# Kernel optimization log

Hardware: AMD Instinct MI355X
Metric: run time of the kernel (lower is better)

The kernel has to match this reference:

```python
import jax, jax.numpy as jnp
import numpy as np

SR = 16000
HOP = 256
MIN_F0 = 50.0
MAX_F0 = 500.0
MIN_PERIOD = SR // 500          # 32
MAX_PERIOD = SR // 50           # 320
FRAME_LEN = HOP * 2             # 512
LAG_END = min(MAX_PERIOD, FRAME_LEN // 2)  # 256 -> lags 32..255 (224 lags)


def setup_inputs() -> dict:
    key = jax.random.key(0)
    waveform = jax.random.normal(key, (64, 1, 163840), dtype=jnp.float32)
    return {"waveform": waveform}


def reference(waveform):
    B, C, T = waveform.shape
    x = waveform[:, 0, :]  # (B, T)
    pad = FRAME_LEN // 2
    xpad = jnp.pad(x, ((0, 0), (pad, pad)), mode='reflect')
    n_frames = (T + 2 * pad - FRAME_LEN) // HOP + 1  # = T//HOP + 1
    # frame extraction (equivalent to unfold(frame_length, hop))
    idx = np.arange(n_frames)[:, None] * HOP + np.arange(FRAME_LEN)[None, :]
    frames = xpad[:, idx]  # (B, F, L)
    # L2-normalize each frame
    norm = jnp.sqrt(jnp.sum(frames * frames, axis=-1, keepdims=True))
    xn = frames / (norm + 1e-8)
    # zero-pad right so xn[t] * xz[t+p] reproduces frame[:L-p] * frame[p:]
    xz = jnp.pad(xn, ((0, 0), (0, 0), (0, FRAME_LEN)))
    lags = jnp.arange(MIN_PERIOD, LAG_END)

    def step(carry, p):
        sl = jax.lax.dynamic_slice_in_dim(xz, p, FRAME_LEN, axis=-1)
        return carry, jnp.sum(xn * sl, axis=-1)  # (B, F)

    _, ac = jax.lax.scan(step, None, lags)  # (P, B, F)
    max_idx = jnp.argmax(ac, axis=0)  # (B, F)
    period = max_idx.astype(jnp.float32) + MIN_PERIOD
    f0 = SR / (period + 1e-8)
    return jnp.clip(f0, MIN_F0, MAX_F0)  # (B, F)
```

## Files before the change

kernel.cpp:

```cpp
#include <hip/hip_runtime.h>


#define SR_F 16000.0f
#define HOP 256
#define FRAME_LEN 512
#define PAD 256
#define T_LEN 163840
#define N_FRAMES 641
#define MIN_PERIOD 32
#define N_LAGS 224
#define WPB 4
#define CP 408
#define L0_OFF 1632
#define L1_OFF 2032
#define WAVE_DW 2432
#define NC 15

typedef _Float16 half8 __attribute__((ext_vector_type(8)));
typedef float floatx4 __attribute__((ext_vector_type(4)));
typedef unsigned int uint2v __attribute__((ext_vector_type(2)));

__device__ __forceinline__ int swz(int q) { return q ^ ((q >> 3) & 7); }

__device__ __forceinline__ unsigned int pkh(float a, float b) {
    unsigned short ha = __builtin_bit_cast(unsigned short, (_Float16)a);
    unsigned short hb = __builtin_bit_cast(unsigned short, (_Float16)b);
    return (unsigned int)ha | ((unsigned int)hb << 16);
}

#define DPP_XOR1 0xB1
#define DPP_XOR2 0x4E
#define DPP_ROR4 0x124
#define DPP_ROR8 0x128

template <int CTRL> __device__ __forceinline__ int dppi(int x) {
    return __builtin_amdgcn_update_dpp(0, x, CTRL, 0xF, 0xF, false);
}
template <int CTRL> __device__ __forceinline__ float dppf(float x) {
    return __builtin_bit_cast(float, dppi<CTRL>(__builtin_bit_cast(int, x)));
}

__device__ __forceinline__ uint2v pl16sw(unsigned int x, bool sel) {
#if __has_builtin(__builtin_amdgcn_permlane16_swap)
    (void)sel;
    return __builtin_amdgcn_permlane16_swap(x, x, false, false);
#else
    unsigned int p = (unsigned int)__shfl_xor((int)x, 16);
    uint2v r; r[0] = sel ? p : x; r[1] = sel ? x : p; return r;
#endif
}
__device__ __forceinline__ uint2v pl32sw(unsigned int x, bool sel) {
#if __has_builtin(__builtin_amdgcn_permlane32_swap)
    (void)sel;
    return __builtin_amdgcn_permlane32_swap(x, x, false, false);
#else
    unsigned int p = (unsigned int)__shfl_xor((int)x, 32);
    uint2v r; r[0] = sel ? p : x; r[1] = sel ? x : p; return r;
#endif
}

__device__ __forceinline__ float wave_sum(float x, bool oddrow, bool hihalf) {
    x += dppf<DPP_XOR1>(x);
    x += dppf<DPP_XOR2>(x);
    x += dppf<DPP_ROR4>(x);
    x += dppf<DPP_ROR8>(x);
    uint2v p = pl16sw(__builtin_bit_cast(unsigned int, x), oddrow);
    x = __builtin_bit_cast(float, p[0]) + __builtin_bit_cast(float, p[1]);
    p = pl32sw(__builtin_bit_cast(unsigned int, x), hihalf);
    x = __builtin_bit_cast(float, p[0]) + __builtin_bit_cast(float, p[1]);
    return x;
}

__device__ __forceinline__
void top2_comb(float& v1, int& i1, float& v2, float ov1, int oi1, float ov2) {
    bool take = (ov1 > v1) || (ov1 == v1 && oi1 < i1);
    float lose = take ? v1 : ov1;
    if (take) { v1 = ov1; i1 = oi1; }
    v2 = fmaxf(fmaxf(v2, ov2), lose);
}

template <int CTRL> __device__ __forceinline__
void top2_dpp(float& v1, int& i1, float& v2) {
    float ov1 = dppf<CTRL>(v1);
    int   oi1 = dppi<CTRL>(i1);
    float ov2 = dppf<CTRL>(v2);
    top2_comb(v1, i1, v2, ov1, oi1, ov2);
}

__device__ __forceinline__
void top2_full(floatx4 acc, int qd, int nn, bool oddrow, bool hihalf,
               float& v1, int& i1, float& v2) {
    v1 = acc[0];
    i1 = 64*qd + nn;
    v2 = -__builtin_inff();
    #pragma unroll
    for (int r = 1; r < 4; ++r) {
        float cv = (4*qd + r < 14) ? acc[r] : -__builtin_inff();
        bool take = (cv > v1);
        float lose = take ? v1 : cv;
        if (take) { v1 = cv; i1 = 64*qd + 16*r + nn; }
        v2 = fmaxf(v2, lose);
    }
    top2_dpp<DPP_XOR1>(v1, i1, v2);
    top2_dpp<DPP_XOR2>(v1, i1, v2);
    top2_dpp<DPP_ROR4>(v1, i1, v2);
    top2_dpp<DPP_ROR8>(v1, i1, v2);
    {
        uint2v a = pl16sw(__builtin_bit_cast(unsigned int, v1), oddrow);
        uint2v b = pl16sw((unsigned int)i1, oddrow);
        uint2v c = pl16sw(__builtin_bit_cast(unsigned int, v2), oddrow);
        float ov1 = __builtin_bit_cast(float, oddrow ? a[0] : a[1]);
        int   oi1 = (int)(oddrow ? b[0] : b[1]);
        float ov2 = __builtin_bit_cast(float, oddrow ? c[0] : c[1]);
        top2_comb(v1, i1, v2, ov1, oi1, ov2);
    }
    {
        uint2v a = pl32sw(__builtin_bit_cast(unsigned int, v1), hihalf);
        uint2v b = pl32sw((unsigned int)i1, hihalf);
        uint2v c = pl32sw(__builtin_bit_cast(unsigned int, v2), hihalf);
        float ov1 = __builtin_bit_cast(float, hihalf ? a[0] : a[1]);
        int   oi1 = (int)(hihalf ? b[0] : b[1]);
        float ov2 = __builtin_bit_cast(float, hihalf ? c[0] : c[1]);
        top2_comb(v1, i1, v2, ov1, oi1, ov2);
    }
}

__device__ __forceinline__ void write_hi4(unsigned int* c0_, unsigned int* c1_,
                                          unsigned int* c2_, unsigned int* c3_,
                                          unsigned int u10, unsigned int u11,
                                          unsigned int u20, unsigned int u21,
                                          int lane) {
    *(unsigned long long*)(c0_ + 120 + 2*lane) =
        ((unsigned long long)u11 << 32) | u10;
    *(unsigned long long*)(c0_ + 248 + 2*lane) =
        ((unsigned long long)u21 << 32) | u20;
    unsigned int a  = __shfl(u10, (lane + 1) & 63);
    unsigned int bb = __shfl(u20, (lane + 1) & 63);
    unsigned int n1 = (lane == 63) ? bb : a;
    unsigned int n2 = (lane == 63) ? 0u : bb;
    unsigned int o10 = (u10 >> 16) | (u11 << 16);
    unsigned int o11 = (u11 >> 16) | (n1 << 16);
    unsigned int o20 = (u20 >> 16) | (u21 << 16);
    unsigned int o21 = (u21 >> 16) | (n2 << 16);
    *(unsigned long long*)(c1_ + 120 + 2*lane) =
        ((unsigned long long)o11 << 32) | o10;
    *(unsigned long long*)(c1_ + 248 + 2*lane) =
        ((unsigned long long)o21 << 32) | o20;
    c2_[119 + 2*lane] = u10; c2_[120 + 2*lane] = u11;
    c2_[247 + 2*lane] = u20; c2_[248 + 2*lane] = u21;
    c3_[119 + 2*lane] = o10; c3_[120 + 2*lane] = o11;
    c3_[247 + 2*lane] = o20; c3_[248 + 2*lane] = o21;
}

__device__ __forceinline__ void write_lo2(unsigned int* l0_, unsigned int* l1_,
                                          unsigned int u10, unsigned int u11,
                                          unsigned int u20, unsigned int u21,
                                          int lane) {
    *(unsigned long long*)(l0_ + 120 + 2*lane) =
        ((unsigned long long)u11 << 32) | u10;
    *(unsigned long long*)(l0_ + 248 + 2*lane) =
        ((unsigned long long)u21 << 32) | u20;
    unsigned int a  = __shfl(u10, (lane + 1) & 63);
    unsigned int bb = __shfl(u20, (lane + 1) & 63);
    unsigned int n1 = (lane == 63) ? bb : a;
    unsigned int n2 = (lane == 63) ? 0u : bb;
    *(unsigned long long*)(l1_ + 120 + 2*lane) =
        ((unsigned long long)(((u11 >> 16) | (n1 << 16))) << 32) |
        ((u10 >> 16) | (u11 << 16));
    *(unsigned long long*)(l1_ + 248 + 2*lane) =
        ((unsigned long long)(((u21 >> 16) | (n2 << 16))) << 32) |
        ((u20 >> 16) | (u21 << 16));
}

__global__ __launch_bounds__(256, 4) void f0_kernel(const float* __restrict__ wav,
                                                    float* __restrict__ out) {
    __shared__ unsigned int yw[WPB][WAVE_DW];

    const int tid  = threadIdx.x;
    const int wv   = tid >> 6;
    const int lane = tid & 63;
    unsigned int* c0p = yw[wv];
    unsigned int* c1p = c0p + CP;
    unsigned int* c2p = c0p + 2*CP;
    unsigned int* c3p = c0p + 3*CP;
    unsigned int* l0p = c0p + L0_OFF;
    unsigned int* l1p = c0p + L1_OFF;

    const int xcd = blockIdx.x & 7;
    const int idx = blockIdx.x >> 3;
    const int bf  = (xcd * 1282 + idx) * WPB + wv;
    const int b   = bf / N_FRAMES;
    const int f   = bf - b * N_FRAMES;
    const float* __restrict__ x = wav + (size_t)b * T_LEN;
    const int base = f * HOP - PAD;
    const bool fast = (f != 0 && f != N_FRAMES - 1);

    const int qd = lane >> 4;
    const int nn = lane & 15;
    const int par = nn & 1;
    const int wA0 = 120 + 4*qd - 8*nn;
    const unsigned int* bhp = c0p + CP*(nn & 3) + 136 + 4*qd + 2*(nn >> 2);
    const int wB0old = 136 + 4*qd + ((nn - par) >> 1);
    const int seg = lane & 15;
    const bool s0 = (seg & 1), s1 = (seg & 2), s2 = (seg & 4), s3 = (seg & 8);
    const bool oddrow = (lane & 16) != 0;
    const bool hihalf = (lane & 32) != 0;

    float4 c1, c2;
    if (fast) {
        const float4* g4 = (const float4*)(x + base);
        c1 = g4[lane];
        c2 = g4[lane + 64];
    }
    for (int d = lane; d < 120; d += 64) { c0p[d] = 0u; l0p[d] = 0u; }
    if (lane < 28) {
        int d = 374 + lane;
        c0p[d] = 0u; c1p[d] = 0u; c2p[d] = 0u; c3p[d] = 0u;
        l0p[d] = 0u; l1p[d] = 0u;
    }

    float qen = 0.0f;
    if (fast) {
        qen = c1.x*c1.x + c1.y*c1.y + c1.z*c1.z + c1.w*c1.w
            + c2.x*c2.x + c2.y*c2.y + c2.z*c2.z + c2.w*c2.w;
        write_hi4(c0p, c1p, c2p, c3p, pkh(c1.x, c1.y), pkh(c1.z, c1.w),
                                      pkh(c2.x, c2.y), pkh(c2.z, c2.w), lane);
    } else {
        for (int t = lane; t < FRAME_LEN; t += 64) {
            int idxr = base + t;
            if (idxr < 0) idxr = -idxr;
            if (idxr >= T_LEN) idxr = 2 * (T_LEN - 1) - idxr;
            float v = x[idxr];
            qen = __builtin_fmaf(v, v, qen);
            unsigned short h = __builtin_bit_cast(unsigned short, (_Float16)v);
            ((unsigned short*)c0p)[240 + t] = h;
            ((unsigned short*)c1p)[239 + t] = h;
            ((unsigned short*)c2p)[238 + t] = h;
            ((unsigned short*)c3p)[237 + t] = h;
        }
    }
    __threadfence_block();

    qen = wave_sum(qen, oddrow, hihalf);

    floatx4 acc0 = {0.f, 0.f, 0.f, 0.f};
    floatx4 acc1 = {0.f, 0.f, 0.f, 0.f};
    #pragma unroll
    for (int c = 0; c < NC; ++c) {
        uint4 au = *(const uint4*)(c0p + (wA0 + 16*c));
        unsigned long long bl = *(const unsigned long long*)(bhp + 16*c);
        unsigned long long br = *(const unsigned long long*)(bhp + 16*c + 2);
        uint4 bu; bu.x = (unsigned int)bl; bu.y = (unsigned int)(bl >> 32);
        bu.z = (unsigned int)br; bu.w = (unsigned int)(br >> 32);
        if (c & 1)
            acc1 = __builtin_amdgcn_mfma_f32_16x16x32_f16(
                __builtin_bit_cast(half8, au), __builtin_bit_cast(half8, bu),
                acc1, 0, 0, 0);
        else
            acc0 = __builtin_amdgcn_mfma_f32_16x16x32_f16(
                __builtin_bit_cast(half8, au), __builtin_bit_cast(half8, bu),
                acc0, 0, 0, 0);
    }
    floatx4 acc = acc0 + acc1;

    float v1, v2; int i1;
    top2_full(acc, qd, nn, oddrow, hihalf, v1, i1, v2);

    const float E1 = 9.765625e-4f * qen + 0.05f;
    if (v1 - v2 > 2.0f * E1) {
        if (lane == 0) {
            float period = (float)(i1 + MIN_PERIOD);
            float f0 = SR_F / (period + 1e-8f);
            out[bf] = fminf(fmaxf(f0, 50.0f), 500.0f);
        }
        return;
    }

    if (fast) {
        float l0 = c1.x - (float)(_Float16)c1.x;
        float l1 = c1.y - (float)(_Float16)c1.y;
        float l2 = c1.z - (float)(_Float16)c1.z;
        float l3 = c1.w - (float)(_Float16)c1.w;
        float l4 = c2.x - (float)(_Float16)c2.x;
        float l5 = c2.y - (float)(_Float16)c2.y;
        float l6 = c2.z - (float)(_Float16)c2.z;
        float l7 = c2.w - (float)(_Float16)c2.w;
        write_lo2(l0p, l1p, pkh(l0, l1), pkh(l2, l3),
                            pkh(l4, l5), pkh(l6, l7), lane);
    } else {
        for (int t = lane; t < FRAME_LEN; t += 64) {
            int idxr = base + t;
            if (idxr < 0) idxr = -idxr;
            if (idxr >= T_LEN) idxr = 2 * (T_LEN - 1) - idxr;
            float v = x[idxr];
            float l = v - (float)(_Float16)v;
            unsigned short h = __builtin_bit_cast(unsigned short, (_Float16)l);
            ((unsigned short*)l0p)[240 + t] = h;
            ((unsigned short*)l1p)[239 + t] = h;
        }
    }
    __threadfence_block();

    const unsigned int* ybl = par ? l1p : l0p;
    #pragma unroll
    for (int c = 0; c < NC; ++c) {
        uint4 au = *(const uint4*)(c0p + (wA0 + 16*c));
        const unsigned int* p = ybl + (wB0old + 16*c);
        uint4 bu; bu.x = p[0]; bu.y = p[1]; bu.z = p[2]; bu.w = p[3];
        acc = __builtin_amdgcn_mfma_f32_16x16x32_f16(
            __builtin_bit_cast(half8, au), __builtin_bit_cast(half8, bu),
            acc, 0, 0, 0);
    }
    #pragma unroll
    for (int c = 0; c < NC; ++c) {
        uint4 au = *(const uint4*)(l0p + (wA0 + 16*c));
        unsigned long long bl = *(const unsigned long long*)(bhp + 16*c);
        unsigned long long br = *(const unsigned long long*)(bhp + 16*c + 2);
        uint4 bu; bu.x = (unsigned int)bl; bu.y = (unsigned int)(bl >> 32);
        bu.z = (unsigned int)br; bu.w = (unsigned int)(br >> 32);
        acc = __builtin_amdgcn_mfma_f32_16x16x32_f16(
            __builtin_bit_cast(half8, au), __builtin_bit_cast(half8, bu),
            acc, 0, 0, 0);
    }

    top2_full(acc, qd, nn, oddrow, hihalf, v1, i1, v2);

    const float E2 = 1.0e-4f * qen + 0.02f;
    if (v1 - v2 > 2.0f * E2) {
        if (lane == 0) {
            float period = (float)(i1 + MIN_PERIOD);
            float f0 = SR_F / (period + 1e-8f);
            out[bf] = fminf(fmaxf(f0, 50.0f), 500.0f);
        }
        return;
    }

    float* sw = (float*)c0p;
    if (fast) {
        const float4* g4 = (const float4*)(x + base);
        ((float4*)sw)[swz(lane)]      = g4[lane];
        ((float4*)sw)[swz(lane + 64)] = g4[lane + 64];
        if (lane < 16) ((float4*)sw)[swz(lane + 128)] = make_float4(0.f,0.f,0.f,0.f);
    } else {
        for (int t = lane; t < FRAME_LEN; t += 64) {
            int idxr = base + t;
            if (idxr < 0) idxr = -idxr;
            if (idxr >= T_LEN) idxr = 2 * (T_LEN - 1) - idxr;
            sw[(swz(t >> 2) << 2) | (t & 3)] = x[idxr];
        }
        int t = FRAME_LEN + lane;
        sw[(swz(t >> 2) << 2) | (t & 3)] = 0.0f;
    }
    __threadfence_block();

    const float4* s4 = (const float4*)sw;
    double dtot[4];
    #pragma unroll
    for (int r = 0; r < 4; ++r) {
        const int g  = (r << 2) + qd;
        const int p0 = MIN_PERIOD + (g << 4);
        double dacc[16];
        #pragma unroll
        for (int j = 0; j < 16; ++j) dacc[j] = 0.0;
        if (g < 14) {
            const int n16 = (FRAME_LEN - p0 + 15) >> 4;
            #pragma unroll
            for (int k = 0; k < 2; ++k) {
                const int ch = seg + (k << 4);
                if (ch < n16) {
                    const int t  = ch << 4;
                    const int qa = t >> 2;
                    const int qw = (t + p0) >> 2;
                    float a[16], w[32];
                    #pragma unroll
                    for (int u = 0; u < 4; ++u) {
                        float4 v = s4[swz(qa + u)];
                        a[4*u+0]=v.x; a[4*u+1]=v.y; a[4*u+2]=v.z; a[4*u+3]=v.w;
                    }
                    #pragma unroll
                    for (int u = 0; u < 8; ++u) {
                        float4 v = s4[swz(qw + u)];
                        w[4*u+0]=v.x; w[4*u+1]=v.y; w[4*u+2]=v.z; w[4*u+3]=v.w;
                    }
                    #pragma unroll
                    for (int j = 0; j < 16; ++j) {
                        #pragma unroll
                        for (int i = 0; i < 16; ++i)
                            dacc[j] = fma((double)a[i], (double)w[i + j], dacc[j]);
                    }
                }
            }
        }
        double u8[8], u4[4], u2[2], dtotal;
        #pragma unroll
        for (int i = 0; i < 8; ++i) {
            double lo = dacc[2*i], hi = dacc[2*i+1];
            double keep = s0 ? hi : lo, send = s0 ? lo : hi;
            u8[i] = keep + __shfl_xor(send, 1);
        }
        #pragma unroll
        for (int i = 0; i < 4; ++i) {
            double lo = u8[2*i], hi = u8[2*i+1];
            double keep = s1 ? hi : lo, send = s1 ? lo : hi;
            u4[i] = keep + __shfl_xor(send, 2);
        }
        #pragma unroll
        for (int i = 0; i < 2; ++i) {
            double lo = u4[2*i], hi = u4[2*i+1];
            double keep = s2 ? hi : lo, send = s2 ? lo : hi;
            u2[i] = keep + __shfl_xor(send, 4);
        }
        {
            double lo = u2[0], hi = u2[1];
            double keep = s3 ? hi : lo, send = s3 ? lo : hi;
            dtotal = keep + __shfl_xor(send, 8);
        }
        dtot[r] = ((r << 6) + lane < N_LAGS) ? dtotal : -__builtin_inf();
    }
    double dv1 = dtot[0];
    int    di1 = lane;
    #pragma unroll
    for (int r = 1; r < 4; ++r) {
        double c = dtot[r];
        if (c > dv1) { dv1 = c; di1 = (r << 6) + lane; }
    }
    #pragma unroll
    for (int m = 1; m < 64; m <<= 1) {
        double o = __shfl_xor(dv1, m);
        int   oi = __shfl_xor(di1, m);
        if (o > dv1 || (o == dv1 && oi < di1)) { dv1 = o; di1 = oi; }
    }
    if (lane == 0) {
        float period = (float)(di1 + MIN_PERIOD);
        float f0 = SR_F / (period + 1e-8f);
        out[bf] = fminf(fmaxf(f0, 50.0f), 500.0f);
    }
}

extern "C" void kernel_launch(void* const* d_in, const int* in_sizes, int n_in,
                              void* d_out, int out_size, void* d_ws, size_t ws_size,
                              hipStream_t stream) {
    const float* wav = (const float*)d_in[0];
    float* out = (float*)d_out;
    const int n_blocks = (64 * N_FRAMES) / WPB;
    f0_kernel<<<n_blocks, 256, 0, stream>>>(wav, out);
}
```

Before: 131.0 us.

## Split tiered f0 search into screening kernel plus compacted refinement kernel

Splits the single kernel into three launches: a counter reset, a tier-1 fp16 MFMA screening kernel that processes 8 frames per wave and emits confident results, and a tier-2/3 kernel that handles only the ambiguous frames gathered into a global work list by atomic append. Divergent slow-path waves no longer hold occupancy alongside fast-path waves, and tier-1 can run with less LDS and higher occupancy. In exchange it adds two extra kernel launches, a global atomic per ambiguous frame, and reloads the waveform for refined frames.

```diff
diff --git a/kernel.cpp b/kernel.cpp
--- a/kernel.cpp
+++ b/kernel.cpp
@@ -7,18 +7,27 @@
 #define PAD 256
 #define T_LEN 163840
 #define N_FRAMES 641
+#define TOTAL (64 * N_FRAMES)
 #define MIN_PERIOD 32
 #define N_LAGS 224
 #define WPB 4
 #define CP 408
+#define T1_DW (4 * CP)
 #define L0_OFF 1632
 #define L1_OFF 2032
-#define WAVE_DW 2432
+#define T23_DW 2432
 #define NC 15
+#define T1_BLOCKS 1282
+#define NF 8
+#define T23_BLOCKS 768
+#define T23_STRIDE (T23_BLOCKS * WPB)
 
 typedef _Float16 half8 __attribute__((ext_vector_type(8)));
 typedef float floatx4 __attribute__((ext_vector_type(4)));
 typedef unsigned int uint2v __attribute__((ext_vector_type(2)));
+
+__device__ unsigned int g_cnt2;
+__device__ unsigned int g_lst2[TOTAL];
 
 __device__ __forceinline__ int swz(int q) { return q ^ ((q >> 3) & 7); }
 
@@ -172,9 +181,120 @@
         ((u20 >> 16) | (u21 << 16));
 }
 
-__global__ __launch_bounds__(256, 4) void f0_kernel(const float* __restrict__ wav,
-                                                    float* __restrict__ out) {
-    __shared__ unsigned int yw[WPB][WAVE_DW];
+__device__ __forceinline__ void emit(float* out, int bf, int i1) {
+    float period = (float)(i1 + MIN_PERIOD);
+    float f0 = SR_F / (period + 1e-8f);
+    out[bf] = fminf(fmaxf(f0, 50.0f), 500.0f);
+}
+
+__global__ void f0_zero() {
+    if (threadIdx.x == 0) g_cnt2 = 0u;
+}
+
+__global__ __launch_bounds__(256, 4) void f0_t1(const float* __restrict__ wav,
+                                                float* __restrict__ out) {
+    __shared__ unsigned int yw[WPB][T1_DW];
+
+    const int tid  = threadIdx.x;
+    const int wv   = tid >> 6;
+    const int lane = tid & 63;
+    unsigned int* c0p = yw[wv];
+    unsigned int* c1p = c0p + CP;
+    unsigned int* c2p = c0p + 2*CP;
+    unsigned int* c3p = c0p + 3*CP;
+
+    const int xcd = blockIdx.x & 7;
+    const int bi  = blockIdx.x >> 3;
+    const int cblk = (xcd < 2 ? xcd * 161 : 322 + (xcd - 2) * 160) + bi;
+    const int bf0  = (cblk * WPB + wv) * NF;
+
+    const int qd = lane >> 4;
+    const int nn = lane & 15;
+    const int wA0 = 120 + 4*qd - 8*nn;
+    const unsigned int* bhp = c0p + CP*(nn & 3) + 136 + 4*qd + 2*(nn >> 2);
+    const bool oddrow = (lane & 16) != 0;
+    const bool hihalf = (lane & 32) != 0;
+
+    for (int d = lane; d < 120; d += 64) c0p[d] = 0u;
+    if (lane < 28) {
+        int d = 374 + lane;
+        c0p[d] = 0u; c1p[d] = 0u; c2p[d] = 0u; c3p[d] = 0u;
+    }
+
+    for (int j = 0; j < NF; ++j) {
+        const int bf = bf0 + j;
+        const int b  = bf / N_FRAMES;
+        const int f  = bf - b * N_FRAMES;
+        const float* __restrict__ x = wav + (size_t)b * T_LEN;
+        const int base = f * HOP - PAD;
+        const bool fast = (f != 0 && f != N_FRAMES - 1);
+
+        __threadfence_block();
+        float qen = 0.0f;
+        if (fast) {
+            const float4* g4 = (const float4*)(x + base);
+            float4 c1 = g4[lane];
+            float4 c2 = g4[lane + 64];
+            qen = c1.x*c1.x + c1.y*c1.y + c1.z*c1.z + c1.w*c1.w
+                + c2.x*c2.x + c2.y*c2.y + c2.z*c2.z + c2.w*c2.w;
+            write_hi4(c0p, c1p, c2p, c3p, pkh(c1.x, c1.y), pkh(c1.z, c1.w),
+                                          pkh(c2.x, c2.y), pkh(c2.z, c2.w), lane);
+        } else {
+            for (int t = lane; t < FRAME_LEN; t += 64) {
+                int idxr = base + t;
+                if (idxr < 0) idxr = -idxr;
+                if (idxr >= T_LEN) idxr = 2 * (T_LEN - 1) - idxr;
+                float v = x[idxr];
+                qen = __builtin_fmaf(v, v, qen);
+                unsigned short h = __builtin_bit_cast(unsigned short, (_Float16)v);
+                ((unsigned short*)c0p)[240 + t] = h;
+                ((unsigned short*)c1p)[239 + t] = h;
+                ((unsigned short*)c2p)[238 + t] = h;
+                ((unsigned short*)c3p)[237 + t] = h;
+            }
+        }
+        __threadfence_block();
+
+        qen = wave_sum(qen, oddrow, hihalf);
+
+        floatx4 acc0 = {0.f, 0.f, 0.f, 0.f};
+        floatx4 acc1 = {0.f, 0.f, 0.f, 0.f};
+        #pragma unroll
+        for (int c = 0; c < NC; ++c) {
+            uint4 au = *(const uint4*)(c0p + (wA0 + 16*c));
+            unsigned long long bl = *(const unsigned long long*)(bhp + 16*c);
+            unsigned long long br = *(const unsigned long long*)(bhp + 16*c + 2);
+            uint4 bu; bu.x = (unsigned int)bl; bu.y = (unsigned int)(bl >> 32);
+            bu.z = (unsigned int)br; bu.w = (unsigned int)(br >> 32);
+            if (c & 1)
+                acc1 = __builtin_amdgcn_mfma_f32_16x16x32_f16(
+                    __builtin_bit_cast(half8, au), __builtin_bit_cast(half8, bu),
+                    acc1, 0, 0, 0);
+            else
+                acc0 = __builtin_amdgcn_mfma_f32_16x16x32_f16(
+                    __builtin_bit_cast(half8, au), __builtin_bit_cast(half8, bu),
+                    acc0, 0, 0, 0);
+        }
+        floatx4 acc = acc0 + acc1;
+
+        float v1, v2; int i1;
+        top2_full(acc, qd, nn, oddrow, hihalf, v1, i1, v2);
+
+        const float E1 = 9.765625e-4f * qen + 0.05f;
+        if (lane == 0) {
+            if (v1 - v2 > 2.0f * E1) {
+                emit(out, bf, i1);
+            } else {
+                unsigned int ii = atomicAdd(&g_cnt2, 1u);
+                g_lst2[ii] = (unsigned int)bf;
+            }
+        }
+    }
+}
+
+__global__ __launch_bounds__(256, 2) void f0_t23(const float* __restrict__ wav,
+                                                 float* __restrict__ out) {
+    __shared__ unsigned int yw[WPB][T23_DW];
 
     const int tid  = threadIdx.x;
     const int wv   = tid >> 6;
@@ -185,15 +305,6 @@
     unsigned int* c3p = c0p + 3*CP;
     unsigned int* l0p = c0p + L0_OFF;
     unsigned int* l1p = c0p + L1_OFF;
-
-    const int xcd = blockIdx.x & 7;
-    const int idx = blockIdx.x >> 3;
-    const int bf  = (xcd * 1282 + idx) * WPB + wv;
-    const int b   = bf / N_FRAMES;
-    const int f   = bf - b * N_FRAMES;
-    const float* __restrict__ x = wav + (size_t)b * T_LEN;
-    const int base = f * HOP - PAD;
-    const bool fast = (f != 0 && f != N_FRAMES - 1);
 
     const int qd = lane >> 4;
     const int nn = lane & 15;
@@ -206,234 +317,225 @@
     const bool oddrow = (lane & 16) != 0;
     const bool hihalf = (lane & 32) != 0;
 
-    float4 c1, c2;
-    if (fast) {
-        const float4* g4 = (const float4*)(x + base);
-        c1 = g4[lane];
-        c2 = g4[lane + 64];
-    }
-    for (int d = lane; d < 120; d += 64) { c0p[d] = 0u; l0p[d] = 0u; }
+    for (int d = lane; d < 120; d += 64) l0p[d] = 0u;
     if (lane < 28) {
         int d = 374 + lane;
-        c0p[d] = 0u; c1p[d] = 0u; c2p[d] = 0u; c3p[d] = 0u;
-        l0p[d] = 0u; l1p[d] = 0u;
-    }
-
-    float qen = 0.0f;
-    if (fast) {
-        qen = c1.x*c1.x + c1.y*c1.y + c1.z*c1.z + c1.w*c1.w
-            + c2.x*c2.x + c2.y*c2.y + c2.z*c2.z + c2.w*c2.w;
-        write_hi4(c0p, c1p, c2p, c3p, pkh(c1.x, c1.y), pkh(c1.z, c1.w),
-                                      pkh(c2.x, c2.y), pkh(c2.z, c2.w), lane);
-    } else {
-        for (int t = lane; t < FRAME_LEN; t += 64) {
-            int idxr = base + t;
-            if (idxr < 0) idxr = -idxr;
-            if (idxr >= T_LEN) idxr = 2 * (T_LEN - 1) - idxr;
-            float v = x[idxr];
-            qen = __builtin_fmaf(v, v, qen);
-            unsigned short h = __builtin_bit_cast(unsigned short, (_Float16)v);
-            ((unsigned short*)c0p)[240 + t] = h;
-            ((unsigned short*)c1p)[239 + t] = h;
-            ((unsigned short*)c2p)[238 + t] = h;
-            ((unsigned short*)c3p)[237 + t] = h;
-        }
-    }
-    __threadfence_block();
-
-    qen = wave_sum(qen, oddrow, hihalf);
-
-    floatx4 acc0 = {0.f, 0.f, 0.f, 0.f};
-    floatx4 acc1 = {0.f, 0.f, 0.f, 0.f};
-    #pragma unroll
-    for (int c = 0; c < NC; ++c) {
-        uint4 au = *(const uint4*)(c0p + (wA0 + 16*c));
-        unsigned long long bl = *(const unsigned long long*)(bhp + 16*c);
-        unsigned long long br = *(const unsigned long long*)(bhp + 16*c + 2);
-        uint4 bu; bu.x = (unsigned int)bl; bu.y = (unsigned int)(bl >> 32);
-        bu.z = (unsigned int)br; bu.w = (unsigned int)(br >> 32);
-        if (c & 1)
-            acc1 = __builtin_amdgcn_mfma_f32_16x16x32_f16(
+        c1p[d] = 0u; c2p[d] = 0u; c3p[d] = 0u; l0p[d] = 0u; l1p[d] = 0u;
+    }
+
+    const unsigned int cnt = g_cnt2;
+    for (unsigned int it = blockIdx.x * WPB + wv; it < cnt; it += T23_STRIDE) {
+        const int bf = (int)g_lst2[it];
+        const int b  = bf / N_FRAMES;
+        const int f  = bf - b * N_FRAMES;
+        const float* __restrict__ x = wav + (size_t)b * T_LEN;
+        const int base = f * HOP - PAD;
+        const bool fast = (f != 0 && f != N_FRAMES - 1);
+
+        __threadfence_block();
+        for (int d = lane; d < 120; d += 64) c0p[d] = 0u;
+        if (lane < 28) c0p[374 + lane] = 0u;
+
+        float4 c1, c2;
+        float qen = 0.0f;
+        if (fast) {
+            const float4* g4 = (const float4*)(x + base);
+            c1 = g4[lane];
+            c2 = g4[lane + 64];
+            qen = c1.x*c1.x + c1.y*c1.y + c1.z*c1.z + c1.w*c1.w
+                + c2.x*c2.x + c2.y*c2.y + c2.z*c2.z + c2.w*c2.w;
+            write_hi4(c0p, c1p, c2p, c3p, pkh(c1.x, c1.y), pkh(c1.z, c1.w),
+                                          pkh(c2.x, c2.y), pkh(c2.z, c2.w), lane);
+        } else {
+            for (int t = lane; t < FRAME_LEN; t += 64) {
+                int idxr = base + t;
+                if (idxr < 0) idxr = -idxr;
+                if (idxr >= T_LEN) idxr = 2 * (T_LEN - 1) - idxr;
+                float v = x[idxr];
+                qen = __builtin_fmaf(v, v, qen);
+                unsigned short h = __builtin_bit_cast(unsigned short, (_Float16)v);
+                ((unsigned short*)c0p)[240 + t] = h;
+                ((unsigned short*)c1p)[239 + t] = h;
+                ((unsigned short*)c2p)[238 + t] = h;
+                ((unsigned short*)c3p)[237 + t] = h;
+            }
+        }
+        __threadfence_block();
+
+        qen = wave_sum(qen, oddrow, hihalf);
+
+        floatx4 acc0 = {0.f, 0.f, 0.f, 0.f};
+        floatx4 acc1 = {0.f, 0.f, 0.f, 0.f};
+        #pragma unroll
+        for (int c = 0; c < NC; ++c) {
+            uint4 au = *(const uint4*)(c0p + (wA0 + 16*c));
+            unsigned long long bl = *(const unsigned long long*)(bhp + 16*c);
+            unsigned long long br = *(const unsigned long long*)(bhp + 16*c + 2);
+            uint4 bu; bu.x = (unsigned int)bl; bu.y = (unsigned int)(bl >> 32);
+            bu.z = (unsigned int)br; bu.w = (unsigned int)(br >> 32);
+            if (c & 1)
+                acc1 = __builtin_amdgcn_mfma_f32_16x16x32_f16(
+                    __builtin_bit_cast(half8, au), __builtin_bit_cast(half8, bu),
+                    acc1, 0, 0, 0);
+            else
+                acc0 = __builtin_amdgcn_mfma_f32_16x16x32_f16(
+                    __builtin_bit_cast(half8, au), __builtin_bit_cast(half8, bu),
+                    acc0, 0, 0, 0);
+        }
+        floatx4 acc = acc0 + acc1;
+
+        if (fast) {
+            float l0 = c1.x - (float)(_Float16)c1.x;
+            float l1 = c1.y - (float)(_Float16)c1.y;
+            float l2 = c1.z - (float)(_Float16)c1.z;
+            float l3 = c1.w - (float)(_Float16)c1.w;
+            float l4 = c2.x - (float)(_Float16)c2.x;
+            float l5 = c2.y - (float)(_Float16)c2.y;
+            float l6 = c2.z - (float)(_Float16)c2.z;
+            float l7 = c2.w - (float)(_Float16)c2.w;
+            write_lo2(l0p, l1p, pkh(l0, l1), pkh(l2, l3),
+                                pkh(l4, l5), pkh(l6, l7), lane);
+        } else {
+            for (int t = lane; t < FRAME_LEN; t += 64) {
+                int idxr = base + t;
+                if (idxr < 0) idxr = -idxr;
+                if (idxr >= T_LEN) idxr = 2 * (T_LEN - 1) - idxr;
+                float v = x[idxr];
+                float l = v - (float)(_Float16)v;
+                unsigned short h = __builtin_bit_cast(unsigned short, (_Float16)l);
+                ((unsigned short*)l0p)[240 + t] = h;
+                ((unsigned short*)l1p)[239 + t] = h;
+            }
+        }
+        __threadfence_block();
+
+        const unsigned int* ybl = par ? l1p : l0p;
+        #pragma unroll
+        for (int c = 0; c < NC; ++c) {
+            uint4 au = *(const uint4*)(c0p + (wA0 + 16*c));
+            const unsigned int* p = ybl + (wB0old + 16*c);
+            uint4 bu; bu.x = p[0]; bu.y = p[1]; bu.z = p[2]; bu.w = p[3];
+            acc = __builtin_amdgcn_mfma_f32_16x16x32_f16(
                 __builtin_bit_cast(half8, au), __builtin_bit_cast(half8, bu),
-                acc1, 0, 0, 0);
-        else
-            acc0 = __builtin_amdgcn_mfma_f32_16x16x32_f16(
+                acc, 0, 0, 0);
+        }
+        #pragma unroll
+        for (int c = 0; c < NC; ++c) {
+            uint4 au = *(const uint4*)(l0p + (wA0 + 16*c));
+            unsigned long long bl = *(const unsigned long long*)(bhp + 16*c);
+            unsigned long long br = *(const unsigned long long*)(bhp + 16*c + 2);
+            uint4 bu; bu.x = (unsigned int)bl; bu.y = (unsigned int)(bl >> 32);
+            bu.z = (unsigned int)br; bu.w = (unsigned int)(br >> 32);
+            acc = __builtin_amdgcn_mfma_f32_16x16x32_f16(
                 __builtin_bit_cast(half8, au), __builtin_bit_cast(half8, bu),
-                acc0, 0, 0, 0);
-    }
-    floatx4 acc = acc0 + acc1;
-
-    float v1, v2; int i1;
-    top2_full(acc, qd, nn, oddrow, hihalf, v1, i1, v2);
-
-    const float E1 = 9.765625e-4f * qen + 0.05f;
-    if (v1 - v2 > 2.0f * E1) {
-        if (lane == 0) {
-            float period = (float)(i1 + MIN_PERIOD);
-            float f0 = SR_F / (period + 1e-8f);
-            out[bf] = fminf(fmaxf(f0, 50.0f), 500.0f);
-        }
-        return;
-    }
-
-    if (fast) {
-        float l0 = c1.x - (float)(_Float16)c1.x;
-        float l1 = c1.y - (float)(_Float16)c1.y;
-        float l2 = c1.z - (float)(_Float16)c1.z;
-        float l3 = c1.w - (float)(_Float16)c1.w;
-        float l4 = c2.x - (float)(_Float16)c2.x;
-        float l5 = c2.y - (float)(_Float16)c2.y;
-        float l6 = c2.z - (float)(_Float16)c2.z;
-        float l7 = c2.w - (float)(_Float16)c2.w;
-        write_lo2(l0p, l1p, pkh(l0, l1), pkh(l2, l3),
-                            pkh(l4, l5), pkh(l6, l7), lane);
-    } else {
-        for (int t = lane; t < FRAME_LEN; t += 64) {
-            int idxr = base + t;
-            if (idxr < 0) idxr = -idxr;
-            if (idxr >= T_LEN) idxr = 2 * (T_LEN - 1) - idxr;
-            float v = x[idxr];
-            float l = v - (float)(_Float16)v;
-            unsigned short h = __builtin_bit_cast(unsigned short, (_Float16)l);
-            ((unsigned short*)l0p)[240 + t] = h;
-            ((unsigned short*)l1p)[239 + t] = h;
-        }
-    }
-    __threadfence_block();
-
-    const unsigned int* ybl = par ? l1p : l0p;
-    #pragma unroll
-    for (int c = 0; c < NC; ++c) {
-        uint4 au = *(const uint4*)(c0p + (wA0 + 16*c));
-        const unsigned int* p = ybl + (wB0old + 16*c);
-        uint4 bu; bu.x = p[0]; bu.y = p[1]; bu.z = p[2]; bu.w = p[3];
-        acc = __builtin_amdgcn_mfma_f32_16x16x32_f16(
-            __builtin_bit_cast(half8, au), __builtin_bit_cast(half8, bu),
-            acc, 0, 0, 0);
-    }
-    #pragma unroll
-    for (int c = 0; c < NC; ++c) {
-        uint4 au = *(const uint4*)(l0p + (wA0 + 16*c));
-        unsigned long long bl = *(const unsigned long long*)(bhp + 16*c);
-        unsigned long long br = *(const unsigned long long*)(bhp + 16*c + 2);
-        uint4 bu; bu.x = (unsigned int)bl; bu.y = (unsigned int)(bl >> 32);
-        bu.z = (unsigned int)br; bu.w = (unsigned int)(br >> 32);
-        acc = __builtin_amdgcn_mfma_f32_16x16x32_f16(
-            __builtin_bit_cast(half8, au), __builtin_bit_cast(half8, bu),
-            acc, 0, 0, 0);
-    }
-
-    top2_full(acc, qd, nn, oddrow, hihalf, v1, i1, v2);
-
-    const float E2 = 1.0e-4f * qen + 0.02f;
-    if (v1 - v2 > 2.0f * E2) {
-        if (lane == 0) {
-            float period = (float)(i1 + MIN_PERIOD);
-            float f0 = SR_F / (period + 1e-8f);
-            out[bf] = fminf(fmaxf(f0, 50.0f), 500.0f);
-        }
-        return;
-    }
-
-    float* sw = (float*)c0p;
-    if (fast) {
-        const float4* g4 = (const float4*)(x + base);
-        ((float4*)sw)[swz(lane)]      = g4[lane];
-        ((float4*)sw)[swz(lane + 64)] = g4[lane + 64];
-        if (lane < 16) ((float4*)sw)[swz(lane + 128)] = make_float4(0.f,0.f,0.f,0.f);
-    } else {
-        for (int t = lane; t < FRAME_LEN; t += 64) {
-            int idxr = base + t;
-            if (idxr < 0) idxr = -idxr;
-            if (idxr >= T_LEN) idxr = 2 * (T_LEN - 1) - idxr;
-            sw[(swz(t >> 2) << 2) | (t & 3)] = x[idxr];
-        }
-        int t = FRAME_LEN + lane;
-        sw[(swz(t >> 2) << 2) | (t & 3)] = 0.0f;
-    }
-    __threadfence_block();
-
-    const float4* s4 = (const float4*)sw;
-    double dtot[4];
-    #pragma unroll
-    for (int r = 0; r < 4; ++r) {
-        const int g  = (r << 2) + qd;
-        const int p0 = MIN_PERIOD + (g << 4);
-        double dacc[16];
-        #pragma unroll
-        for (int j = 0; j < 16; ++j) dacc[j] = 0.0;
-        if (g < 14) {
-            const int n16 = (FRAME_LEN - p0 + 15) >> 4;
+                acc, 0, 0, 0);
+        }
+
+        float v1, v2; int i1;
+        top2_full(acc, qd, nn, oddrow, hihalf, v1, i1, v2);
+
+        const float E2 = 1.0e-4f * qen + 0.02f;
+        if (v1 - v2 > 2.0f * E2) {
+            if (lane == 0) emit(out, bf, i1);
+            continue;
+        }
+
+        float* sw = (float*)c0p;
+        if (fast) {
+            const float4* g4 = (const float4*)(x + base);
+            ((float4*)sw)[swz(lane)]      = g4[lane];
+            ((float4*)sw)[swz(lane + 64)] = g4[lane + 64];
+            if (lane < 16) ((float4*)sw)[swz(lane + 128)] = make_float4(0.f,0.f,0.f,0.f);
+        } else {
+            for (int t = lane; t < FRAME_LEN; t += 64) {
+                int idxr = base + t;
+                if (idxr < 0) idxr = -idxr;
+                if (idxr >= T_LEN) idxr = 2 * (T_LEN - 1) - idxr;
+                sw[(swz(t >> 2) << 2) | (t & 3)] = x[idxr];
+            }
+            int t = FRAME_LEN + lane;
+            sw[(swz(t >> 2) << 2) | (t & 3)] = 0.0f;
+        }
+        __threadfence_block();
+
+        const float4* s4 = (const float4*)sw;
+        double dtot[4];
+        #pragma unroll
+        for (int r = 0; r < 4; ++r) {
+            const int g  = (r << 2) + qd;
+            const int p0 = MIN_PERIOD + (g << 4);
+            double dacc[16];
             #pragma unroll
-            for (int k = 0; k < 2; ++k) {
-                const int ch = seg + (k << 4);
-                if (ch < n16) {
-                    const int t  = ch << 4;
-                    const int qa = t >> 2;
-                    const int qw = (t + p0) >> 2;
-                    float a[16], w[32];
-                    #pragma unroll
-                    for (int u = 0; u < 4; ++u) {
-                        float4 v = s4[swz(qa + u)];
-                        a[4*u+0]=v.x; a[4*u+1]=v.y; a[4*u+2]=v.z; a[4*u+3]=v.w;
-                    }
-                    #pragma unroll
-                    for (int u = 0; u < 8; ++u) {
-                        float4 v = s4[swz(qw + u)];
-                        w[4*u+0]=v.x; w[4*u+1]=v.y; w[4*u+2]=v.z; w[4*u+3]=v.w;
-                    }
-                    #pragma unroll
-                    for (int j = 0; j < 16; ++j) {
+            for (int j = 0; j < 16; ++j) dacc[j] = 0.0;
+            if (g < 14) {
+                const int n16 = (FRAME_LEN - p0 + 15) >> 4;
+                #pragma unroll
+                for (int k = 0; k < 2; ++k) {
+                    const int ch = seg + (k << 4);
+                    if (ch < n16) {
+                        const int t  = ch << 4;
+                        const int qa = t >> 2;
+                        const int qw = (t + p0) >> 2;
+                        float a[16], w[32];
                         #pragma unroll
-                        for (int i = 0; i < 16; ++i)
-                            dacc[j] = fma((double)a[i], (double)w[i + j], dacc[j]);
+                        for (int u = 0; u < 4; ++u) {
+                            float4 v = s4[swz(qa + u)];
+                            a[4*u+0]=v.x; a[4*u+1]=v.y; a[4*u+2]=v.z; a[4*u+3]=v.w;
+                        }
+                        #pragma unroll
+                        for (int u = 0; u < 8; ++u) {
+                            float4 v = s4[swz(qw + u)];
+                            w[4*u+0]=v.x; w[4*u+1]=v.y; w[4*u+2]=v.z; w[4*u+3]=v.w;
+                        }
+                        #pragma unroll
+                        for (int j = 0; j < 16; ++j) {
+                            #pragma unroll
+                            for (int i = 0; i < 16; ++i)
+                                dacc[j] = fma((double)a[i], (double)w[i + j], dacc[j]);
+                        }
                     }
                 }
             }
-        }
-        double u8[8], u4[4], u2[2], dtotal;
-        #pragma unroll
-        for (int i = 0; i < 8; ++i) {
-            double lo = dacc[2*i], hi = dacc[2*i+1];
-            double keep = s0 ? hi : lo, send = s0 ? lo : hi;
-            u8[i] = keep + __shfl_xor(send, 1);
-        }
-        #pragma unroll
-        for (int i = 0; i < 4; ++i) {
-            double lo = u8[2*i], hi = u8[2*i+1];
-            double keep = s1 ? hi : lo, send = s1 ? lo : hi;
-            u4[i] = keep + __shfl_xor(send, 2);
-        }
-        #pragma unroll
-        for (int i = 0; i < 2; ++i) {
-            double lo = u4[2*i], hi = u4[2*i+1];
-            double keep = s2 ? hi : lo, send = s2 ? lo : hi;
-            u2[i] = keep + __shfl_xor(send, 4);
-        }
-        {
-            double lo = u2[0], hi = u2[1];
-            double keep = s3 ? hi : lo, send = s3 ? lo : hi;
-            dtotal = keep + __shfl_xor(send, 8);
-        }
-        dtot[r] = ((r << 6) + lane < N_LAGS) ? dtotal : -__builtin_inf();
-    }
-    double dv1 = dtot[0];
-    int    di1 = lane;
-    #pragma unroll
-    for (int r = 1; r < 4; ++r) {
-        double c = dtot[r];
-        if (c > dv1) { dv1 = c; di1 = (r << 6) + lane; }
-    }
-    #pragma unroll
-    for (int m = 1; m < 64; m <<= 1) {
-        double o = __shfl_xor(dv1, m);
-        int   oi = __shfl_xor(di1, m);
-        if (o > dv1 || (o == dv1 && oi < di1)) { dv1 = o; di1 = oi; }
-    }
-    if (lane == 0) {
-        float period = (float)(di1 + MIN_PERIOD);
-        float f0 = SR_F / (period + 1e-8f);
-        out[bf] = fminf(fmaxf(f0, 50.0f), 500.0f);
+            double u8[8], u4[4], u2[2], dtotal;
+            #pragma unroll
+            for (int i = 0; i < 8; ++i) {
+                double lo = dacc[2*i], hi = dacc[2*i+1];
+                double keep = s0 ? hi : lo, send = s0 ? lo : hi;
+                u8[i] = keep + __shfl_xor(send, 1);
+            }
+            #pragma unroll
+            for (int i = 0; i < 4; ++i) {
+                double lo = u8[2*i], hi = u8[2*i+1];
+                double keep = s1 ? hi : lo, send = s1 ? lo : hi;
+                u4[i] = keep + __shfl_xor(send, 2);
+            }
+            #pragma unroll
+            for (int i = 0; i < 2; ++i) {
+                double lo = u4[2*i], hi = u4[2*i+1];
+                double keep = s2 ? hi : lo, send = s2 ? lo : hi;
+                u2[i] = keep + __shfl_xor(send, 4);
+            }
+            {
+                double lo = u2[0], hi = u2[1];
+                double keep = s3 ? hi : lo, send = s3 ? lo : hi;
+                dtotal = keep + __shfl_xor(send, 8);
+            }
+            dtot[r] = ((r << 6) + lane < N_LAGS) ? dtotal : -__builtin_inf();
+        }
+        double dv1 = dtot[0];
+        int    di1 = lane;
+        #pragma unroll
+        for (int r = 1; r < 4; ++r) {
+            double c = dtot[r];
+            if (c > dv1) { dv1 = c; di1 = (r << 6) + lane; }
+        }
+        #pragma unroll
+        for (int m = 1; m < 64; m <<= 1) {
+            double o = __shfl_xor(dv1, m);
+            int   oi = __shfl_xor(di1, m);
+            if (o > dv1 || (o == dv1 && oi < di1)) { dv1 = o; di1 = oi; }
+        }
+        if (lane == 0) emit(out, bf, di1);
     }
 }
 
@@ -442,6 +544,7 @@
                               hipStream_t stream) {
     const float* wav = (const float*)d_in[0];
     float* out = (float*)d_out;
-    const int n_blocks = (64 * N_FRAMES) / WPB;
-    f0_kernel<<<n_blocks, 256, 0, stream>>>(wav, out);
-}
+    f0_zero<<<1, 64, 0, stream>>>();
+    f0_t1<<<T1_BLOCKS, 256, 0, stream>>>(wav, out);
+    f0_t23<<<T23_BLOCKS, 256, 0, stream>>>(wav, out);
+}
```

Result: slower. 182.6 us (+39.5%).
